# Performance work log

Hardware: AMD Instinct MI355X
Metric: run time of the kernel (lower is better)

Reference implementation:

```python
import jax, jax.numpy as jnp
import numpy as np

D_MODEL = 384
H = 12
HEAD_DIM = D_MODEL // H
# Faithful to source: scale = (d_model // h) ** (-5)  (likely a typo for -0.5, but we match the code)
SCALE = float(HEAD_DIM) ** (-5.0)


def setup_inputs() -> dict:
    key = jax.random.key(0)
    ks = jax.random.split(key, 6)
    B, N, D = 4096, 49, D_MODEL
    x = jax.random.normal(ks[0], (B, N, D), dtype=jnp.float32)
    mask = jnp.zeros((B, 1, N, N), dtype=jnp.float32)
    s = 1.0 / np.sqrt(D)
    Wq = jax.random.normal(ks[1], (D, D), dtype=jnp.float32) * s
    Wk = jax.random.normal(ks[2], (D, D), dtype=jnp.float32) * s
    Wv = jax.random.normal(ks[3], (D, D), dtype=jnp.float32) * s
    Wp = jax.random.normal(ks[4], (D, D), dtype=jnp.float32) * s
    bq = jnp.zeros((D,), jnp.float32)
    bk = jnp.zeros((D,), jnp.float32)
    bv = jnp.zeros((D,), jnp.float32)
    bp = jnp.zeros((D,), jnp.float32)
    return {"x": x, "mask": mask, "Wq": Wq, "bq": bq, "Wk": Wk, "bk": bk,
            "Wv": Wv, "bv": bv, "Wp": Wp, "bp": bp}


def reference(x, mask, Wq, bq, Wk, bk, Wv, bv, Wp, bp):
    # x: [B, N, D] where B = batch*num_windows, N = window_size**2
    B, N, D = x.shape
    def heads(y):  # [B,N,D] -> [B,H,N,hd]
        return y.reshape(B, N, H, HEAD_DIM).transpose(0, 2, 1, 3)
    q = heads(x @ Wq + bq)
    k = heads(x @ Wk + bk)
    v = heads(x @ Wv + bv)
    scores = jnp.einsum('bhnd,bhmd->bhnm', q, k) * SCALE + mask  # mask broadcasts over heads
    w = jax.nn.softmax(scores, axis=-1)  # dropout=0 -> identity
    o = jnp.einsum('bhnm,bhmd->bhnd', w, v)
    o = o.transpose(0, 2, 1, 3).reshape(B, N, D)
    return o @ Wp + bp
```

## Files before the change

kernel.cpp:

```cpp
#include <hip/hip_runtime.h>


#define NWIN   4096
#define NTOK   49
#define DMODEL 384
#define NH     12
#define HD     32
#define XPITCH 392
#define QP     40
#define VP     72
#define SCALE  2.9802322387695312e-08f
#define NEGBIG -30000.0f

#define S_BASE 19208
#define S_STR  6224
#define LDS_TOT 31656

typedef __attribute__((ext_vector_type(8)))  short short8;
typedef __attribute__((ext_vector_type(4)))  short short4v;
typedef __attribute__((ext_vector_type(4)))  float float4v;
typedef __attribute__((ext_vector_type(16))) float float16v;

__device__ __align__(16) unsigned short g_wT[4 * DMODEL * DMODEL];
__device__ int g_dt;

__device__ __forceinline__ float b2f(unsigned short h) {
  union { unsigned u; float f; } t; t.u = ((unsigned)h) << 16; return t.f;
}
__device__ __forceinline__ unsigned short f2b(float f) {
  union { float f; unsigned u; } t; t.f = f;
  return (unsigned short)((t.u + 0x7fffu + ((t.u >> 16) & 1u)) >> 16);
}
__device__ __forceinline__ unsigned cvt_pk_bf16(float lo, float hi) {
  unsigned r;
  asm("v_cvt_pk_bf16_f32 %0, %1, %2" : "=v"(r) : "v"(lo), "v"(hi));
  return r;
}

__global__ void detect_dtype(const unsigned short* __restrict__ x) {
  __shared__ int cnt;
  if (threadIdx.x == 0) cnt = 0;
  __syncthreads();
  int local = 0;
  for (int i = threadIdx.x; i < 2048; i += 256) {
    unsigned short h = x[2 * i];
    int e = (h >> 7) & 0xFF;
    if (e >= 0x6A && e <= 0x90) local++;
  }
  atomicAdd(&cnt, local);
  __syncthreads();
  if (threadIdx.x == 0) g_dt = (cnt < 1024) ? 1 : 0;
}

__global__ void prep_weights(const void* __restrict__ Wq,
                             const void* __restrict__ Wk,
                             const void* __restrict__ Wv,
                             const void* __restrict__ Wp) {
  int o = blockIdx.x * 256 + threadIdx.x;
  int e = o & 511;
  int t = o >> 9;
  int l = e >> 3, j = e & 7;
  int k, col;
  const void* W;
  if (t < 864) {
    int h = t / 72, r = t - h * 72;
    int ks = r / 3, mat = r - ks * 3;
    W = (mat == 0) ? Wq : (mat == 1) ? Wk : Wv;
    k = ks * 16 + (l >> 5) * 8 + j;
    col = h * 32 + (l & 31);
  } else {
    int tp = t - 864;
    int wv = tp / 72, r = tp - wv * 72;
    int ks = r / 6, nt = r - ks * 6;
    W = Wp;
    k = ks * 32 + (l >> 4) * 8 + j;
    col = wv * 96 + nt * 16 + (l & 15);
  }
  unsigned short v;
  if (g_dt) v = f2b(((const float*)W)[k * DMODEL + col]);
  else      v = ((const unsigned short*)W)[k * DMODEL + col];
  g_wT[o] = v;
}

#define BAR() do {                                          \
    asm volatile("s_waitcnt lgkmcnt(0)" ::: "memory");      \
    __builtin_amdgcn_s_barrier();                           \
    asm volatile("" ::: "memory");                          \
  } while (0)

#define MFMA32(A, B, C) __builtin_amdgcn_mfma_f32_32x32x16_bf16((A), (B), (C), 0, 0, 0)
#define MFMA16(A, B, C) __builtin_amdgcn_mfma_f32_16x16x32_bf16((A), (B), (C), 0, 0, 0)

__global__ __launch_bounds__(256, 2)
void win_attn(const void* __restrict__ xg_,
              const void* __restrict__ maskg_,
              const void* __restrict__ bqg_,
              const void* __restrict__ bkg_,
              const void* __restrict__ bvg_,
              const void* __restrict__ bpg_,
              void* __restrict__ outg_)
{
  __shared__ __align__(16) short lds[LDS_TOT];
  const int dt   = g_dt;
  const int win  = blockIdx.x;
  const int tid  = threadIdx.x;
  const int wv   = tid >> 6;
  const int lane = tid & 63;
  const int cl   = lane & 31;
  const int hi   = lane >> 5;
  const int c    = lane & 15;
  const int qd   = lane >> 4;
  const int b    = wv & 1;
  const int h2   = wv >> 1;

  const unsigned short* const wl = g_wT + lane * 8;

  short8 wb[12];
  {
    const unsigned short* w0 = wl + (h2 * 72) * 512;
    #pragma unroll
    for (int t = 0; t < 12; ++t) wb[t] = *(const short8*)(w0 + t * 512);
  }

  {
    unsigned* z = (unsigned*)&lds[S_BASE];
    for (int i = tid; i < 6224; i += 256) z[i] = 0u;
  }

  if (dt == 0) {
    const uint4* src = (const uint4*)((const unsigned short*)xg_ + (size_t)win * (NTOK * DMODEL));
    for (int i = tid; i < (NTOK * DMODEL) / 8; i += 256) {
      int row = i / 48, col = i - row * 48;
      *(uint4*)&lds[row * XPITCH + col * 8] = src[i];
    }
  } else {
    const float4* src = (const float4*)((const float*)xg_ + (size_t)win * (NTOK * DMODEL));
    for (int i = tid; i < (NTOK * DMODEL) / 4; i += 256) {
      int row = i / 96, colq = i - row * 96;
      float4 f = src[i];
      short4v p;
      p[0] = (short)f2b(f.x); p[1] = (short)f2b(f.y);
      p[2] = (short)f2b(f.z); p[3] = (short)f2b(f.w);
      *(short4v*)&lds[row * XPITCH + colq * 4] = p;
    }
  }

  short* const sQh = lds + S_BASE + h2 * S_STR;
  short* const sKh = sQh + 1960;
  short* const sVt = sQh + 3920;
  short* const sO  = lds;

  unsigned maddpk[16];
  {
    int qrow = b * 32 + cl; if (qrow > NTOK - 1) qrow = NTOK - 1;
    const size_t mb = (size_t)win * (NTOK * NTOK) + (size_t)qrow * NTOK;
    #pragma unroll
    for (int kt = 0; kt < 2; ++kt)
      #pragma unroll
      for (int i = 0; i < 8; ++i) {
        int k0 = kt * 32 + ((2 * i) & 3) + 8 * ((2 * i) >> 2) + 4 * hi;
        float m0 = (k0     < NTOK)
          ? (dt ? ((const float*)maskg_)[mb + k0]     : b2f(((const unsigned short*)maskg_)[mb + k0]))
          : NEGBIG;
        float m1 = (k0 + 1 < NTOK)
          ? (dt ? ((const float*)maskg_)[mb + k0 + 1] : b2f(((const unsigned short*)maskg_)[mb + k0 + 1]))
          : NEGBIG;
        maddpk[kt * 8 + i] = cvt_pk_bf16(m0, m1);
      }
  }

  BAR();

  short8 xa[24];
  {
    const int xrow = b * 32 + cl;
    const int xr   = (xrow < NTOK) ? xrow : 0;
    const short8 z8 = {0, 0, 0, 0, 0, 0, 0, 0};
    #pragma unroll
    for (int ks = 0; ks < 24; ++ks) {
      short8 t = *(const short8*)&lds[xr * XPITCH + ks * 16 + hi * 8];
      xa[ks] = (xrow < NTOK) ? t : z8;
    }
  }

  const float4v z4 = {0.f, 0.f, 0.f, 0.f};

  #pragma unroll 1
  for (int p = 0; p < 6; ++p) {
    const int h = 2 * p + h2;
    const unsigned short* const wh = wl + h * 72 * 512;

    const int colh = h * 32 + cl;
    const float biasQ = dt ? ((const float*)bqg_)[colh] : b2f(((const unsigned short*)bqg_)[colh]);
    const float biasK = dt ? ((const float*)bkg_)[colh] : b2f(((const unsigned short*)bkg_)[colh]);
    const float biasV = dt ? ((const float*)bvg_)[colh] : b2f(((const unsigned short*)bvg_)[colh]);

    float16v aQ, aK, aV;
    #pragma unroll
    for (int i = 0; i < 16; ++i) { aQ[i] = 0.f; aK[i] = 0.f; aV[i] = 0.f; }
    #pragma unroll
    for (int ks = 0; ks < 24; ++ks) {
      const int s = (ks & 3) * 3;
      const short8 a = xa[ks];
      aQ = MFMA32(a, wb[s + 0], aQ);
      aK = MFMA32(a, wb[s + 1], aK);
      aV = MFMA32(a, wb[s + 2], aV);
      const unsigned short* pf;
      if (ks < 20)      pf = wh + ((ks + 4) * 3) * 512;
      else if (p < 5)   pf = wh + (144 + (ks - 20) * 3) * 512;
      else              pf = g_wT + 442368 + wv * 36864 + lane * 8 + ((ks - 20) * 3) * 512;
      wb[s + 0] = *(const short8*)(pf + 0 * 512);
      wb[s + 1] = *(const short8*)(pf + 1 * 512);
      wb[s + 2] = *(const short8*)(pf + 2 * 512);
    }

    #pragma unroll
    for (int i = 0; i < 16; ++i) {
      const int tok = (i & 3) + 8 * (i >> 2) + 4 * hi + b * 32;
      if (tok < NTOK) {
        sQh[tok * QP + cl] = (short)f2b(aQ[i] + biasQ);
        sKh[tok * QP + cl] = (short)f2b(aK[i] + biasK);
      }
    }
    #pragma unroll
    for (int i = 0; i < 8; ++i) {
      const int tok = ((2 * i) & 3) + 8 * ((2 * i) >> 2) + 4 * hi + b * 32;
      if (tok < NTOK) {
        float v0 = aV[2 * i] + biasV;
        float v1 = (tok + 1 < NTOK) ? (aV[2 * i + 1] + biasV) : 0.f;
        *(unsigned*)&sVt[cl * VP + tok] = cvt_pk_bf16(v0, v1);
      }
    }
    BAR();

    float16v S0, S1;
    #pragma unroll
    for (int i = 0; i < 16; ++i) { S0[i] = 0.f; S1[i] = 0.f; }
    {
      int qr  = b * 32 + cl; if (qr > NTOK - 1) qr = NTOK - 1;
      const int kr0 = cl;
      int kr1 = 32 + cl; if (kr1 > NTOK - 1) kr1 = NTOK - 1;
      #pragma unroll
      for (int ks = 0; ks < 2; ++ks) {
        const short8 qf  = *(const short8*)&sQh[qr  * QP + ks * 16 + hi * 8];
        const short8 kf0 = *(const short8*)&sKh[kr0 * QP + ks * 16 + hi * 8];
        const short8 kf1 = *(const short8*)&sKh[kr1 * QP + ks * 16 + hi * 8];
        S0 = MFMA32(kf0, qf, S0);
        S1 = MFMA32(kf1, qf, S1);
      }
    }

    float w32[32];
    #pragma unroll
    for (int kt = 0; kt < 2; ++kt)
      #pragma unroll
      for (int i = 0; i < 8; ++i) {
        const unsigned pk = maddpk[kt * 8 + i];
        const float m0 = __uint_as_float(pk << 16);
        const float m1 = __uint_as_float(pk & 0xffff0000u);
        const float sv0 = kt ? S1[2 * i]     : S0[2 * i];
        const float sv1 = kt ? S1[2 * i + 1] : S0[2 * i + 1];
        w32[kt * 16 + 2 * i]     = fmaf(sv0, SCALE, m0);
        w32[kt * 16 + 2 * i + 1] = fmaf(sv1, SCALE, m1);
      }
    float t16[16], t8[8], t4[4];
    #pragma unroll
    for (int i = 0; i < 16; ++i) t16[i] = fmaxf(w32[2 * i], w32[2 * i + 1]);
    #pragma unroll
    for (int i = 0; i < 8; ++i)  t8[i] = fmaxf(t16[2 * i], t16[2 * i + 1]);
    #pragma unroll
    for (int i = 0; i < 4; ++i)  t4[i] = fmaxf(t8[2 * i], t8[2 * i + 1]);
    float mx = fmaxf(fmaxf(t4[0], t4[1]), fmaxf(t4[2], t4[3]));
    mx = fmaxf(mx, __shfl_xor(mx, 32));
    #pragma unroll
    for (int i = 0; i < 32; ++i) w32[i] = __expf(w32[i] - mx);
    #pragma unroll
    for (int i = 0; i < 16; ++i) t16[i] = w32[2 * i] + w32[2 * i + 1];
    #pragma unroll
    for (int i = 0; i < 8; ++i)  t8[i] = t16[2 * i] + t16[2 * i + 1];
    #pragma unroll
    for (int i = 0; i < 4; ++i)  t4[i] = t8[2 * i] + t8[2 * i + 1];
    float sum = (t4[0] + t4[1]) + (t4[2] + t4[3]);
    sum += __shfl_xor(sum, 32);
    const float inv = 1.0f / sum;
    #pragma unroll
    for (int i = 0; i < 32; ++i) w32[i] *= inv;

    unsigned pw[16];
    #pragma unroll
    for (int i = 0; i < 16; ++i)
      pw[i] = cvt_pk_bf16(w32[2 * i], w32[2 * i + 1]);
    short8 pa[4];
    #pragma unroll
    for (int ks = 0; ks < 4; ++ks) {
      const unsigned q0 = pw[ks * 4 + 0], q1 = pw[ks * 4 + 1];
      const unsigned q2 = pw[ks * 4 + 2], q3 = pw[ks * 4 + 3];
      const unsigned t0 = hi ? q0 : q2;
      const unsigned t1 = hi ? q1 : q3;
      const unsigned x0 = __shfl_xor(t0, 32);
      const unsigned x1 = __shfl_xor(t1, 32);
      union { unsigned u[4]; short8 s; } u;
      u.u[0] = hi ? x0 : q0;
      u.u[1] = hi ? x1 : q1;
      u.u[2] = hi ? q2 : x0;
      u.u[3] = hi ? q3 : x1;
      pa[ks] = u.s;
    }

    float16v aO;
    #pragma unroll
    for (int i = 0; i < 16; ++i) aO[i] = 0.f;
    #pragma unroll
    for (int ks = 0; ks < 4; ++ks) {
      const short8 bv8 = *(const short8*)&sVt[cl * VP + ks * 16 + hi * 8];
      aO = MFMA32(pa[ks], bv8, aO);
    }

    #pragma unroll
    for (int i = 0; i < 16; ++i) {
      const int tok = (i & 3) + 8 * (i >> 2) + 4 * hi + b * 32;
      if (tok < NTOK)
        sO[tok * XPITCH + h * 32 + cl] = (short)f2b(aO[i]);
    }
    BAR();
  }

  const unsigned short* const wp = g_wT + 442368 + wv * 36864 + lane * 8;

  float biasP[6];
  #pragma unroll
  for (int nt = 0; nt < 6; ++nt) {
    const int col = wv * 96 + nt * 16 + c;
    biasP[nt] = dt ? ((const float*)bpg_)[col] : b2f(((const unsigned short*)bpg_)[col]);
  }

  float4v aP[4][6];
  #pragma unroll
  for (int mt = 0; mt < 4; ++mt)
    #pragma unroll
    for (int nt = 0; nt < 6; ++nt) aP[mt][nt] = z4;

  short8 af[2][4];
  #pragma unroll
  for (int mt = 0; mt < 4; ++mt) {
    int row = mt * 16 + c; if (row > NTOK - 1) row = NTOK - 1;
    af[0][mt] = *(const short8*)&sO[row * XPITCH + qd * 8];
  }

  #pragma unroll
  for (int ks = 0; ks < 12; ++ks) {
    const int cs = ks & 1;
    if (ks < 11) {
      #pragma unroll
      for (int mt = 0; mt < 4; ++mt) {
        int row = mt * 16 + c; if (row > NTOK - 1) row = NTOK - 1;
        af[cs ^ 1][mt] = *(const short8*)&sO[row * XPITCH + (ks + 1) * 32 + qd * 8];
      }
    }
    const int s = cs * 6;
    #pragma unroll
    for (int nt = 0; nt < 6; ++nt) {
      aP[0][nt] = MFMA16(af[cs][0], wb[s + nt], aP[0][nt]);
      aP[1][nt] = MFMA16(af[cs][1], wb[s + nt], aP[1][nt]);
      aP[2][nt] = MFMA16(af[cs][2], wb[s + nt], aP[2][nt]);
      aP[3][nt] = MFMA16(af[cs][3], wb[s + nt], aP[3][nt]);
      if (ks < 10) wb[s + nt] = *(const short8*)(wp + ((ks + 2) * 6 + nt) * 512);
    }
  }

  #pragma unroll
  for (int nt = 0; nt < 6; ++nt) {
    const int col = wv * 96 + nt * 16 + c;
    #pragma unroll
    for (int mt = 0; mt < 4; ++mt) {
      #pragma unroll
      for (int r = 0; r < 4; ++r) {
        const int m = mt * 16 + qd * 4 + r;
        if (m < NTOK) {
          const float v = aP[mt][nt][r] + biasP[nt];
          const size_t off = (size_t)win * (NTOK * DMODEL) + m * DMODEL + col;
          if (dt) ((float*)outg_)[off] = v;
          else    ((unsigned short*)outg_)[off] = f2b(v);
        }
      }
    }
  }
}

extern "C" void kernel_launch(void* const* d_in, const int* in_sizes, int n_in,
                              void* d_out, int out_size, void* d_ws, size_t ws_size,
                              hipStream_t stream) {
  const void* x    = d_in[0];
  const void* mask = d_in[1];
  const void* Wq   = d_in[2];
  const void* bq   = d_in[3];
  const void* Wk   = d_in[4];
  const void* bk   = d_in[5];
  const void* Wv   = d_in[6];
  const void* bv   = d_in[7];
  const void* Wp   = d_in[8];
  const void* bp   = d_in[9];

  detect_dtype<<<1, 256, 0, stream>>>((const unsigned short*)x);
  prep_weights<<<(4 * DMODEL * DMODEL) / 256, 256, 0, stream>>>(Wq, Wk, Wv, Wp);
  win_attn<<<NWIN, 256, 0, stream>>>(x, mask, bq, bk, bv, bp, d_out);
}
```

Measured before the change: 1.009 ms.

## Software-pipeline QKV projection of next head with softmax/PV of current head

Restructures the per-head loop so the QKV projection MFMAs for the next head pair run between the score computation and the softmax/PV of the current head. The intent is to overlap independent matrix and vector work and hide LDS and barrier latency. It also defers softmax normalization to a single multiply on the PV output rather than scaling all 32 weights. The cost is higher register pressure from holding both score and QKV accumulators live, plus an extra barrier per iteration.

```diff
diff --git a/kernel.cpp b/kernel.cpp
--- a/kernel.cpp
+++ b/kernel.cpp
@@ -114,6 +114,7 @@
   const int h2   = wv >> 1;
 
   const unsigned short* const wl = g_wT + lane * 8;
+  const unsigned short* const wp = g_wT + 442368 + wv * 36864 + lane * 8;
 
   short8 wb[12];
   {
@@ -183,73 +184,63 @@
     }
   }
 
-  const float4v z4 = {0.f, 0.f, 0.f, 0.f};
-
-  #pragma unroll 1
-  for (int p = 0; p < 6; ++p) {
-    const int h = 2 * p + h2;
-    const unsigned short* const wh = wl + h * 72 * 512;
-
-    const int colh = h * 32 + cl;
-    const float biasQ = dt ? ((const float*)bqg_)[colh] : b2f(((const unsigned short*)bqg_)[colh]);
-    const float biasK = dt ? ((const float*)bkg_)[colh] : b2f(((const unsigned short*)bkg_)[colh]);
-    const float biasV = dt ? ((const float*)bvg_)[colh] : b2f(((const unsigned short*)bvg_)[colh]);
-
-    float16v aQ, aK, aV;
-    #pragma unroll
-    for (int i = 0; i < 16; ++i) { aQ[i] = 0.f; aK[i] = 0.f; aV[i] = 0.f; }
+  auto qkv_pass = [&](const unsigned short* whn, const unsigned short* pfNext,
+                      float16v& q, float16v& k, float16v& v) {
+    #pragma unroll
+    for (int i = 0; i < 16; ++i) { q[i] = 0.f; k[i] = 0.f; v[i] = 0.f; }
     #pragma unroll
     for (int ks = 0; ks < 24; ++ks) {
       const int s = (ks & 3) * 3;
       const short8 a = xa[ks];
-      aQ = MFMA32(a, wb[s + 0], aQ);
-      aK = MFMA32(a, wb[s + 1], aK);
-      aV = MFMA32(a, wb[s + 2], aV);
-      const unsigned short* pf;
-      if (ks < 20)      pf = wh + ((ks + 4) * 3) * 512;
-      else if (p < 5)   pf = wh + (144 + (ks - 20) * 3) * 512;
-      else              pf = g_wT + 442368 + wv * 36864 + lane * 8 + ((ks - 20) * 3) * 512;
+      q = MFMA32(a, wb[s + 0], q);
+      k = MFMA32(a, wb[s + 1], k);
+      v = MFMA32(a, wb[s + 2], v);
+      const unsigned short* pf = (ks < 20) ? (whn + ((ks + 4) * 3) * 512)
+                                           : (pfNext + ((ks - 20) * 3) * 512);
       wb[s + 0] = *(const short8*)(pf + 0 * 512);
       wb[s + 1] = *(const short8*)(pf + 1 * 512);
       wb[s + 2] = *(const short8*)(pf + 2 * 512);
     }
-
+  };
+
+  auto qkv_store = [&](const float16v& q, const float16v& k, const float16v& v,
+                       float bQ, float bK, float bV) {
     #pragma unroll
     for (int i = 0; i < 16; ++i) {
       const int tok = (i & 3) + 8 * (i >> 2) + 4 * hi + b * 32;
       if (tok < NTOK) {
-        sQh[tok * QP + cl] = (short)f2b(aQ[i] + biasQ);
-        sKh[tok * QP + cl] = (short)f2b(aK[i] + biasK);
+        sQh[tok * QP + cl] = (short)f2b(q[i] + bQ);
+        sKh[tok * QP + cl] = (short)f2b(k[i] + bK);
       }
     }
     #pragma unroll
     for (int i = 0; i < 8; ++i) {
       const int tok = ((2 * i) & 3) + 8 * ((2 * i) >> 2) + 4 * hi + b * 32;
       if (tok < NTOK) {
-        float v0 = aV[2 * i] + biasV;
-        float v1 = (tok + 1 < NTOK) ? (aV[2 * i + 1] + biasV) : 0.f;
+        float v0 = v[2 * i] + bV;
+        float v1 = (tok + 1 < NTOK) ? (v[2 * i + 1] + bV) : 0.f;
         *(unsigned*)&sVt[cl * VP + tok] = cvt_pk_bf16(v0, v1);
       }
     }
-    BAR();
-
-    float16v S0, S1;
+  };
+
+  auto scores = [&](float16v& S0, float16v& S1) {
     #pragma unroll
     for (int i = 0; i < 16; ++i) { S0[i] = 0.f; S1[i] = 0.f; }
-    {
-      int qr  = b * 32 + cl; if (qr > NTOK - 1) qr = NTOK - 1;
-      const int kr0 = cl;
-      int kr1 = 32 + cl; if (kr1 > NTOK - 1) kr1 = NTOK - 1;
-      #pragma unroll
-      for (int ks = 0; ks < 2; ++ks) {
-        const short8 qf  = *(const short8*)&sQh[qr  * QP + ks * 16 + hi * 8];
-        const short8 kf0 = *(const short8*)&sKh[kr0 * QP + ks * 16 + hi * 8];
-        const short8 kf1 = *(const short8*)&sKh[kr1 * QP + ks * 16 + hi * 8];
-        S0 = MFMA32(kf0, qf, S0);
-        S1 = MFMA32(kf1, qf, S1);
-      }
-    }
-
+    int qr  = b * 32 + cl; if (qr > NTOK - 1) qr = NTOK - 1;
+    const int kr0 = cl;
+    int kr1 = 32 + cl; if (kr1 > NTOK - 1) kr1 = NTOK - 1;
+    #pragma unroll
+    for (int ks = 0; ks < 2; ++ks) {
+      const short8 qf  = *(const short8*)&sQh[qr  * QP + ks * 16 + hi * 8];
+      const short8 kf0 = *(const short8*)&sKh[kr0 * QP + ks * 16 + hi * 8];
+      const short8 kf1 = *(const short8*)&sKh[kr1 * QP + ks * 16 + hi * 8];
+      S0 = MFMA32(kf0, qf, S0);
+      S1 = MFMA32(kf1, qf, S1);
+    }
+  };
+
+  auto softmax_pv_store = [&](int h, const float16v& S0, const float16v& S1) {
     float w32[32];
     #pragma unroll
     for (int kt = 0; kt < 2; ++kt)
@@ -283,8 +274,6 @@
     float sum = (t4[0] + t4[1]) + (t4[2] + t4[3]);
     sum += __shfl_xor(sum, 32);
     const float inv = 1.0f / sum;
-    #pragma unroll
-    for (int i = 0; i < 32; ++i) w32[i] *= inv;
 
     unsigned pw[16];
     #pragma unroll
@@ -320,20 +309,61 @@
     for (int i = 0; i < 16; ++i) {
       const int tok = (i & 3) + 8 * (i >> 2) + 4 * hi + b * 32;
       if (tok < NTOK)
-        sO[tok * XPITCH + h * 32 + cl] = (short)f2b(aO[i]);
-    }
+        sO[tok * XPITCH + h * 32 + cl] = (short)f2b(aO[i] * inv);
+    }
+  };
+
+  auto load_bias = [&](const void* bg, int col) -> float {
+    return dt ? ((const float*)bg)[col] : b2f(((const unsigned short*)bg)[col]);
+  };
+
+  float16v qA, kA, vA;
+  {
+    const int hn = h2;
+    const float bQ = load_bias(bqg_, hn * 32 + cl);
+    const float bK = load_bias(bkg_, hn * 32 + cl);
+    const float bV = load_bias(bvg_, hn * 32 + cl);
+    qkv_pass(wl + hn * 72 * 512, wl + (hn + 2) * 72 * 512, qA, kA, vA);
+    qkv_store(qA, kA, vA, bQ, bK, bV);
+  }
+  BAR();
+
+  #pragma unroll 1
+  for (int p = 0; p < 5; ++p) {
+    const int h  = 2 * p + h2;
+    const int hn = h + 2;
+    const float bQ = load_bias(bqg_, hn * 32 + cl);
+    const float bK = load_bias(bkg_, hn * 32 + cl);
+    const float bV = load_bias(bvg_, hn * 32 + cl);
+
+    float16v S0, S1;
+    scores(S0, S1);
+
+    const unsigned short* pfNext = (p == 4) ? wp : (wl + (hn + 2) * 72 * 512);
+    qkv_pass(wl + hn * 72 * 512, pfNext, qA, kA, vA);
+    softmax_pv_store(h, S0, S1);
+
     BAR();
-  }
-
-  const unsigned short* const wp = g_wT + 442368 + wv * 36864 + lane * 8;
+    qkv_store(qA, kA, vA, bQ, bK, bV);
+    BAR();
+  }
+
+  {
+    const int h = 10 + h2;
+    float16v S0, S1;
+    scores(S0, S1);
+    softmax_pv_store(h, S0, S1);
+  }
+  BAR();
 
   float biasP[6];
   #pragma unroll
   for (int nt = 0; nt < 6; ++nt) {
     const int col = wv * 96 + nt * 16 + c;
-    biasP[nt] = dt ? ((const float*)bpg_)[col] : b2f(((const unsigned short*)bpg_)[col]);
-  }
-
+    biasP[nt] = load_bias(bpg_, col);
+  }
+
+  const float4v z4 = {0.f, 0.f, 0.f, 0.f};
   float4v aP[4][6];
   #pragma unroll
   for (int mt = 0; mt < 4; ++mt)
```

New measurement: 1.189 ms. 1.18x slower.
